# Optimization experiments

Measured on AMD Instinct MI355X. Metric: run time of the kernel, lower is better.

The kernel has to match this reference:

```python
import jax, jax.numpy as jnp
import numpy as np

B, T, E, H = 8, 4096, 1024, 128

def setup_inputs() -> dict:
    key = jax.random.key(0)
    kx, kq, kk, kv = jax.random.split(key, 4)
    x = jax.random.normal(kx, (B, T, E), dtype=jnp.float32)
    # bias-free Linear weights stored as (in, out) for x @ W
    scale = 1.0 / np.sqrt(E)
    Wq = jax.random.normal(kq, (E, H), dtype=jnp.float32) * scale
    Wk = jax.random.normal(kk, (E, H), dtype=jnp.float32) * scale
    Wv = jax.random.normal(kv, (E, H), dtype=jnp.float32) * scale
    return {"x": x, "Wq": Wq, "Wk": Wk, "Wv": Wv}

def reference(x, Wq, Wk, Wv):
    # x: (B,T,E) -> out: (B,T,H). Causal single-head attention, dropout p=0 (no-op).
    q = x @ Wq  # (B,T,H)
    k = x @ Wk
    v = x @ Wv
    head_norm = jnp.sqrt(jnp.float32(q.shape[-1]))
    att = jnp.einsum('bth,bsh->bts', q, k) / head_norm  # (B,T,T)
    causal = jnp.tril(jnp.ones((x.shape[1], x.shape[1]), dtype=bool))
    att = jnp.where(causal, att, -jnp.inf)
    att = jax.nn.softmax(att, axis=-1)
    return jnp.einsum('bts,bsh->bth', att, v)
```

## Files before the change

### kernel.cpp

```cpp
#include <hip/hip_runtime.h>
#include <hip/hip_bf16.h>
#include <stdint.h>

#define Bn 8
#define Tn 4096
#define En 1024
#define Hn 128
#define SCALE 0.08838834764831845f

typedef __attribute__((ext_vector_type(8))) short bf16x8;
typedef __attribute__((ext_vector_type(4))) float f32x4;

__device__ __forceinline__ float bf2f(unsigned short v) {
    return __uint_as_float(((unsigned int)v) << 16);
}
__device__ __forceinline__ unsigned int pkbf(float a, float b) {
    __hip_bfloat162 h = __float22bfloat162_rn(make_float2(a, b));
    union { __hip_bfloat162 h2; unsigned int u; } cv;
    cv.h2 = h;
    return cv.u;
}

__device__ __forceinline__ void gll16(const unsigned short* g, unsigned short* l) {
    __builtin_amdgcn_global_load_lds(
        (const __attribute__((address_space(1))) void*)g,
        (__attribute__((address_space(3))) void*)l, 16, 0, 0);
}

__global__ __launch_bounds__(256)
void qkv_mfma(const float* __restrict__ x,
              const float* __restrict__ Wq,
              const float* __restrict__ Wk,
              const float* __restrict__ Wv,
              unsigned short* __restrict__ Qo,
              unsigned short* __restrict__ Ko,
              unsigned short* __restrict__ Vo) {
    const int mt = blockIdx.x;
    const int which = blockIdx.y;
    const float* W = (which == 0) ? Wq : (which == 1) ? Wk : Wv;
    unsigned short* out = (which == 0) ? Qo : (which == 1) ? Ko : Vo;
    const float scale = (which == 0) ? SCALE : 1.0f;

    __shared__ alignas(16) unsigned short Xs[128 * 72];
    __shared__ alignas(16) unsigned short Wt[128 * 72];

    const int t = threadIdx.x;
    const int w = t >> 6;
    const int lane = t & 63;
    const int quad = lane >> 4;
    const int l16 = lane & 15;

    const int xrow = t >> 1;
    const int xkc = (t & 1) * 32;
    const int ws0 = (t & 31) * 2;
    const int wd0 = (t >> 5) * 16;

    const float* xsrc0 = x + (size_t)(mt * 128 + xrow) * En + xkc;

    f32x4 acc[2][8];
#pragma unroll
    for (int mi = 0; mi < 2; ++mi)
#pragma unroll
        for (int nst = 0; nst < 8; ++nst) acc[mi][nst] = (f32x4){0.f, 0.f, 0.f, 0.f};

    float4 xpre[8], wpre[8];
    {
        const float* src = xsrc0;
#pragma unroll
        for (int i = 0; i < 8; ++i) xpre[i] = *(const float4*)(src + i * 4);
        const float* w0 = W + (size_t)ws0 * Hn + wd0;
        const float* w1 = w0 + Hn;
#pragma unroll
        for (int i = 0; i < 4; ++i) wpre[i] = *(const float4*)(w0 + i * 4);
#pragma unroll
        for (int i = 0; i < 4; ++i) wpre[4 + i] = *(const float4*)(w1 + i * 4);
    }

    for (int kt = 0; kt < 16; ++kt) {
        __syncthreads();
        {
            unsigned int u[16];
#pragma unroll
            for (int i = 0; i < 8; ++i) {
                u[2 * i]     = pkbf(xpre[i].x, xpre[i].y);
                u[2 * i + 1] = pkbf(xpre[i].z, xpre[i].w);
            }
#pragma unroll
            for (int i = 0; i < 4; ++i)
                *(uint4*)&Xs[xrow * 72 + xkc + i * 8] = ((const uint4*)u)[i];

            const float* ax = (const float*)&wpre[0];
            const float* bx = (const float*)&wpre[4];
#pragma unroll
            for (int dd = 0; dd < 16; ++dd)
                *(unsigned int*)&Wt[(wd0 + dd) * 72 + ws0] = pkbf(ax[dd], bx[dd]);
        }
        if (kt < 15) {
            const float* src = xsrc0 + (kt + 1) * 64;
#pragma unroll
            for (int i = 0; i < 8; ++i) xpre[i] = *(const float4*)(src + i * 4);
            const float* w0 = W + (size_t)((kt + 1) * 64 + ws0) * Hn + wd0;
            const float* w1 = w0 + Hn;
#pragma unroll
            for (int i = 0; i < 4; ++i) wpre[i] = *(const float4*)(w0 + i * 4);
#pragma unroll
            for (int i = 0; i < 4; ++i) wpre[4 + i] = *(const float4*)(w1 + i * 4);
        }
        __syncthreads();

#pragma unroll
        for (int ks = 0; ks < 2; ++ks) {
            bf16x8 af[2];
#pragma unroll
            for (int mi = 0; mi < 2; ++mi)
                af[mi] = *(const bf16x8*)&Xs[(w * 32 + mi * 16 + l16) * 72 + ks * 32 + quad * 8];
#pragma unroll
            for (int nst = 0; nst < 8; ++nst) {
                bf16x8 bfr = *(const bf16x8*)&Wt[(nst * 16 + l16) * 72 + ks * 32 + quad * 8];
                acc[0][nst] = __builtin_amdgcn_mfma_f32_16x16x32_bf16(bfr, af[0], acc[0][nst], 0, 0, 0);
                acc[1][nst] = __builtin_amdgcn_mfma_f32_16x16x32_bf16(bfr, af[1], acc[1][nst], 0, 0, 0);
            }
        }
    }

#pragma unroll
    for (int mi = 0; mi < 2; ++mi) {
        const size_t rowbase = (size_t)(mt * 128 + w * 32 + mi * 16 + l16) * Hn;
#pragma unroll
        for (int nst = 0; nst < 8; ++nst) {
            f32x4 v = acc[mi][nst];
            uint2 pk;
            pk.x = pkbf(v[0] * scale, v[1] * scale);
            pk.y = pkbf(v[2] * scale, v[3] * scale);
            *(uint2*)(out + rowbase + nst * 16 + quad * 4) = pk;
        }
    }
}

#define KSWZ(r, c) (((r) << 8) + ((c) ^ (((r) & 7) << 4)))
#define VSWZ(r, c) (((r) << 7) + ((c) ^ (((r) & 7) << 4)))

__global__ __launch_bounds__(512, 4)
void flash_mfma(const unsigned short* __restrict__ Qb,
                const unsigned short* __restrict__ Kb,
                const unsigned short* __restrict__ Vb,
                float* __restrict__ out) {
    const int b = blockIdx.x;
    const int bx = blockIdx.y;
    const int qt = (bx < 32) ? (63 - bx) : (bx - 32);
    const int t = threadIdx.x;
    const int w = t >> 6;
    const int g = w >> 2;
    const int rg = w & 3;
    const int lane = t & 63;
    const int quad = lane >> 4;
    const int l16 = lane & 15;
    const int t256 = t & 255;

    extern __shared__ unsigned short pool[];
    char* const poolb = (char*)pool;
    char* const Kg = poolb + g * 16384;
    char* const Vg = poolb + 32768 + g * 16384;
    char* const Pw = poolb + 65536 + w * 2048;
    float* const Os = (float*)poolb;
    float* const Ex = (float*)(poolb + 40960);
    float* const Em = (float*)(poolb + 73728);
    float* const El = Em + 64;

    const size_t gbase = (size_t)b * ((size_t)Tn * Hn);
    const unsigned short* kbase = Kb + gbase;
    const unsigned short* vbase = Vb + gbase;

    const int l_hi = lane >> 4;
    const int cpr = (lane & 15) * 16;
    const int vs0 = (t256 & 31) * 2;
    const int vd0 = (t256 >> 5) * 16;

    uint4 vra, vrb, vrc, vrd;
    if (g <= qt) {
        const unsigned short* vsrc = vbase + (size_t)(g * 64) * Hn;
        vra = *(const uint4*)&vsrc[vs0 * 128 + vd0];
        vrb = *(const uint4*)&vsrc[vs0 * 128 + vd0 + 8];
        vrc = *(const uint4*)&vsrc[(vs0 + 1) * 128 + vd0];
        vrd = *(const uint4*)&vsrc[(vs0 + 1) * 128 + vd0 + 8];
    }

    {
        const unsigned short* qsrc = Qb + gbase + (size_t)(qt * 64) * Hn;
#pragma unroll
        for (int i = 0; i < 2; ++i) {
            const int row = w * 8 + i * 4 + l_hi;
            const int scol = cpr ^ ((row & 7) << 4);
            gll16(qsrc + row * 128 + (scol >> 1),
                  (unsigned short*)(poolb + w * 2048 + i * 1024));
        }
    }
    __syncthreads();

    bf16x8 qf[4];
#pragma unroll
    for (int ks = 0; ks < 4; ++ks)
        qf[ks] = *(const bf16x8*)(poolb + KSWZ(rg * 16 + l16, ks * 64 + quad * 16));

    f32x4 acc_o[8];
#pragma unroll
    for (int i = 0; i < 8; ++i) acc_o[i] = (f32x4){0.f, 0.f, 0.f, 0.f};
    float m_run = -1e30f, l_run = 0.f;

    const int n = (qt >> 1) + 1;
    for (int it = 0; it < n; ++it) {
        const int kt = 2 * it + g;
        const bool active = (kt <= qt);
        __syncthreads();
        if (active) {
            const unsigned short* ktile = kbase + (size_t)(kt * 64) * Hn;
#pragma unroll
            for (int i = 0; i < 4; ++i) {
                const int row = rg * 16 + i * 4 + l_hi;
                const int scol = cpr ^ ((row & 7) << 4);
                gll16(ktile + row * 128 + (scol >> 1),
                      (unsigned short*)(Kg + rg * 4096 + i * 1024));
            }
            const unsigned short* pa = (const unsigned short*)&vra;
            const unsigned short* pb = (const unsigned short*)&vrb;
            const unsigned short* pc = (const unsigned short*)&vrc;
            const unsigned short* pd = (const unsigned short*)&vrd;
#pragma unroll
            for (int dd = 0; dd < 8; ++dd)
                *(unsigned int*)(Vg + VSWZ(vd0 + dd, vs0 * 2)) =
                    (unsigned int)pa[dd] | ((unsigned int)pc[dd] << 16);
#pragma unroll
            for (int dd = 0; dd < 8; ++dd)
                *(unsigned int*)(Vg + VSWZ(vd0 + 8 + dd, vs0 * 2)) =
                    (unsigned int)pb[dd] | ((unsigned int)pd[dd] << 16);
        }
        __syncthreads();
        if (kt + 2 <= qt) {
            const unsigned short* vsrc = vbase + (size_t)((kt + 2) * 64) * Hn;
            vra = *(const uint4*)&vsrc[vs0 * 128 + vd0];
            vrb = *(const uint4*)&vsrc[vs0 * 128 + vd0 + 8];
            vrc = *(const uint4*)&vsrc[(vs0 + 1) * 128 + vd0];
            vrd = *(const uint4*)&vsrc[(vs0 + 1) * 128 + vd0 + 8];
        }
        if (!active) continue;

        const bool diag = (kt == qt);
        f32x4 sa[4];
#pragma unroll
        for (int st = 0; st < 4; ++st) {
            if (diag && st > rg) {
                sa[st] = (f32x4){-1e30f, -1e30f, -1e30f, -1e30f};
            } else {
                f32x4 c = (f32x4){0.f, 0.f, 0.f, 0.f};
#pragma unroll
                for (int ks = 0; ks < 4; ++ks) {
                    bf16x8 kf = *(const bf16x8*)(Kg + KSWZ(st * 16 + l16, ks * 64 + quad * 16));
                    c = __builtin_amdgcn_mfma_f32_16x16x32_bf16(kf, qf[ks], c, 0, 0, 0);
                }
                if (diag && st == rg) {
#pragma unroll
                    for (int r = 0; r < 4; ++r)
                        if (quad * 4 + r > l16) c[r] = -1e30f;
                }
                sa[st] = c;
            }
        }

        float mloc = -1e30f;
#pragma unroll
        for (int st = 0; st < 4; ++st)
#pragma unroll
            for (int r = 0; r < 4; ++r) mloc = fmaxf(mloc, sa[st][r]);
        mloc = fmaxf(mloc, __shfl_xor(mloc, 16));
        mloc = fmaxf(mloc, __shfl_xor(mloc, 32));
        const float m_new = fmaxf(m_run, mloc);
        const float alpha = __expf(m_run - m_new);
        float lsum = 0.f;
#pragma unroll
        for (int st = 0; st < 4; ++st)
#pragma unroll
            for (int r = 0; r < 4; ++r) {
                const float e = __expf(sa[st][r] - m_new);
                sa[st][r] = e;
                lsum += e;
            }
        lsum += __shfl_xor(lsum, 16);
        lsum += __shfl_xor(lsum, 32);
        l_run = l_run * alpha + lsum;
        m_run = m_new;
#pragma unroll
        for (int i = 0; i < 8; ++i) acc_o[i] *= alpha;

#pragma unroll
        for (int st = 0; st < 4; ++st) {
            uint2 pk;
            pk.x = pkbf(sa[st][0], sa[st][1]);
            pk.y = pkbf(sa[st][2], sa[st][3]);
            *(uint2*)(Pw + VSWZ(l16, st * 32 + quad * 8)) = pk;
        }
        bf16x8 pf0 = *(const bf16x8*)(Pw + VSWZ(l16, quad * 16));
        bf16x8 pf1 = *(const bf16x8*)(Pw + VSWZ(l16, 64 + quad * 16));

#pragma unroll
        for (int dt = 0; dt < 8; ++dt) {
            bf16x8 vf0 = *(const bf16x8*)(Vg + VSWZ(dt * 16 + l16, quad * 16));
            acc_o[dt] = __builtin_amdgcn_mfma_f32_16x16x32_bf16(vf0, pf0, acc_o[dt], 0, 0, 0);
            bf16x8 vf1 = *(const bf16x8*)(Vg + VSWZ(dt * 16 + l16, 64 + quad * 16));
            acc_o[dt] = __builtin_amdgcn_mfma_f32_16x16x32_bf16(vf1, pf1, acc_o[dt], 0, 0, 0);
        }
    }

    __syncthreads();
    if (g == 1) {
        float* dst = Ex + (rg * 16 + l16) * 128;
#pragma unroll
        for (int dt = 0; dt < 8; ++dt)
            *(f32x4*)&dst[dt * 16 + quad * 4] = acc_o[dt];
        if (quad == 0) {
            Em[rg * 16 + l16] = m_run;
            El[rg * 16 + l16] = l_run;
        }
    }
    __syncthreads();
    if (g == 0) {
        const float* src = Ex + (rg * 16 + l16) * 128;
        const float m2 = Em[rg * 16 + l16];
        const float l2 = El[rg * 16 + l16];
        const float ms = fmaxf(m_run, m2);
        const float a1 = __expf(m_run - ms);
        const float a2 = __expf(m2 - ms);
        const float linv = 1.f / (l_run * a1 + l2 * a2);
#pragma unroll
        for (int dt = 0; dt < 8; ++dt) {
            f32x4 o2 = *(const f32x4*)&src[dt * 16 + quad * 4];
            f32x4 v = (acc_o[dt] * a1 + o2 * a2) * linv;
            *(f32x4*)&Os[(rg * 16 + l16) * 132 + dt * 16 + quad * 4] = v;
        }
    }
    __syncthreads();
    float* dst = out + gbase + (size_t)(qt * 64) * Hn;
#pragma unroll
    for (int i = 0; i < 4; ++i) {
        const int idx = (t + i * 512) * 4;
        const int row = idx >> 7, col = idx & 127;
        *(float4*)&dst[row * 128 + col] = *(const float4*)&Os[row * 132 + col];
    }
}

extern "C" void kernel_launch(void* const* d_in, const int* in_sizes, int n_in,
                              void* d_out, int out_size, void* d_ws, size_t ws_size,
                              hipStream_t stream) {
    const float* x  = (const float*)d_in[0];
    const float* Wq = (const float*)d_in[1];
    const float* Wk = (const float*)d_in[2];
    const float* Wv = (const float*)d_in[3];
    float* o = (float*)d_out;

    unsigned short* Qb = (unsigned short*)d_ws;
    unsigned short* Kb = Qb + (size_t)Bn * Tn * Hn;
    unsigned short* Vb = Kb + (size_t)Bn * Tn * Hn;

    static bool attr_done = false;
    if (!attr_done) {
        hipFuncSetAttribute((const void*)flash_mfma,
                            hipFuncAttributeMaxDynamicSharedMemorySize, 81920);
        attr_done = true;
    }

    qkv_mfma<<<dim3(256, 3), 256, 0, stream>>>(x, Wq, Wk, Wv, Qb, Kb, Vb);
    flash_mfma<<<dim3(8, 64), 512, 81920, stream>>>(Qb, Kb, Vb, o);
}
```

Baseline: 369.8 us.

## Pre-convert x and weights to bf16 and use pipelined LDS-staged QKV GEMM

Adds separate kernels that convert x to bf16 and convert/transpose the projection weights once. A new QKV GEMM then reads bf16 tiles via direct global-to-LDS loads with XOR swizzle and double buffering. This is meant to cut redundant fp32 loads and in-kernel conversion across the three projection blocks, at the cost of an extra pass writing a bf16 copy of x, extra launches, and a larger workspace requirement with fallback to the old path.

```diff
diff --git a/kernel.cpp b/kernel.cpp
--- a/kernel.cpp
+++ b/kernel.cpp
@@ -25,6 +25,137 @@
     __builtin_amdgcn_global_load_lds(
         (const __attribute__((address_space(1))) void*)g,
         (__attribute__((address_space(3))) void*)l, 16, 0, 0);
+}
+
+__global__ __launch_bounds__(256)
+void xcvt(const float* __restrict__ x, unsigned short* __restrict__ xb) {
+    const size_t i = ((size_t)blockIdx.x * 256 + threadIdx.x) * 16;
+    const float4* src = (const float4*)(x + i);
+    float4 a = src[0], b = src[1], c = src[2], d = src[3];
+    uint4 o0, o1;
+    o0.x = pkbf(a.x, a.y); o0.y = pkbf(a.z, a.w);
+    o0.z = pkbf(b.x, b.y); o0.w = pkbf(b.z, b.w);
+    o1.x = pkbf(c.x, c.y); o1.y = pkbf(c.z, c.w);
+    o1.z = pkbf(d.x, d.y); o1.w = pkbf(d.z, d.w);
+    *(uint4*)(xb + i) = o0;
+    *(uint4*)(xb + i + 8) = o1;
+}
+
+__global__ __launch_bounds__(256)
+void wcvt(const float* __restrict__ Wq, const float* __restrict__ Wk,
+          const float* __restrict__ Wv, unsigned short* __restrict__ wt3) {
+    const int which = blockIdx.x;
+    const int k0 = blockIdx.y * 128;
+    const float* W = (which == 0) ? Wq : (which == 1) ? Wk : Wv;
+    unsigned short* wt = wt3 + (size_t)which * 131072;
+
+    __shared__ unsigned short wl[128 * 132];
+    const int t = threadIdx.x;
+#pragma unroll
+    for (int i = 0; i < 16; ++i) {
+        const int idx = t + i * 256;
+        const int k = idx >> 5, c4 = idx & 31;
+        float4 v = *(const float4*)&W[(size_t)(k0 + k) * Hn + c4 * 4];
+        uint2 p;
+        p.x = pkbf(v.x, v.y);
+        p.y = pkbf(v.z, v.w);
+        *(uint2*)&wl[k * 132 + c4 * 4] = p;
+    }
+    __syncthreads();
+#pragma unroll
+    for (int j = 0; j < 32; ++j) {
+        const int idx = t + j * 256;
+        const int n = idx >> 6, kp = idx & 63;
+        unsigned int u = (unsigned int)wl[(2 * kp) * 132 + n] |
+                         ((unsigned int)wl[(2 * kp + 1) * 132 + n] << 16);
+        *(unsigned int*)&wt[(size_t)n * 1024 + k0 + 2 * kp] = u;
+    }
+}
+
+#define QSWZ(r, c) (((r) << 7) + ((c) ^ (((r) & 7) << 4)))
+
+__global__ __launch_bounds__(256)
+void qkv2(const unsigned short* __restrict__ xb,
+          const unsigned short* __restrict__ wt3,
+          unsigned short* __restrict__ Qo,
+          unsigned short* __restrict__ Ko,
+          unsigned short* __restrict__ Vo) {
+    const int mt = blockIdx.x;
+    const int which = blockIdx.y;
+    const unsigned short* wt = wt3 + (size_t)which * 131072;
+    unsigned short* out = (which == 0) ? Qo : (which == 1) ? Ko : Vo;
+    const float scale = (which == 0) ? SCALE : 1.0f;
+
+    __shared__ alignas(16) unsigned short Xs[2][128 * 64];
+    __shared__ alignas(16) unsigned short Ws[2][128 * 64];
+
+    const int t = threadIdx.x;
+    const int w = t >> 6;
+    const int lane = t & 63;
+    const int quad = lane >> 4;
+    const int l16 = lane & 15;
+    const int r8 = lane >> 3;
+    const int cb = lane & 7;
+
+    const unsigned short* xtile = xb + (size_t)(mt * 128) * En;
+
+    f32x4 acc[2][8];
+#pragma unroll
+    for (int mi = 0; mi < 2; ++mi)
+#pragma unroll
+        for (int nst = 0; nst < 8; ++nst) acc[mi][nst] = (f32x4){0.f, 0.f, 0.f, 0.f};
+
+    auto stage = [&](int buf, int kt) {
+#pragma unroll
+        for (int i = 0; i < 4; ++i) {
+            const int row = i * 32 + w * 8 + r8;
+            gll16(xtile + (size_t)row * En + kt * 64 + ((cb ^ (row & 7)) * 8),
+                  &Xs[buf][(i * 32 + w * 8) * 64]);
+        }
+#pragma unroll
+        for (int i = 0; i < 4; ++i) {
+            const int row = i * 32 + w * 8 + r8;
+            gll16(wt + (size_t)row * 1024 + kt * 64 + ((cb ^ (row & 7)) * 8),
+                  &Ws[buf][(i * 32 + w * 8) * 64]);
+        }
+    };
+
+    stage(0, 0);
+    __syncthreads();
+
+    for (int kt = 0; kt < 16; ++kt) {
+        const int buf = kt & 1;
+        if (kt < 15) stage(buf ^ 1, kt + 1);
+        const char* xs = (const char*)Xs[buf];
+        const char* ws = (const char*)Ws[buf];
+#pragma unroll
+        for (int ks = 0; ks < 2; ++ks) {
+            bf16x8 af[2];
+#pragma unroll
+            for (int mi = 0; mi < 2; ++mi)
+                af[mi] = *(const bf16x8*)(xs + QSWZ(w * 32 + mi * 16 + l16, ks * 64 + quad * 16));
+#pragma unroll
+            for (int nst = 0; nst < 8; ++nst) {
+                bf16x8 bfr = *(const bf16x8*)(ws + QSWZ(nst * 16 + l16, ks * 64 + quad * 16));
+                acc[0][nst] = __builtin_amdgcn_mfma_f32_16x16x32_bf16(bfr, af[0], acc[0][nst], 0, 0, 0);
+                acc[1][nst] = __builtin_amdgcn_mfma_f32_16x16x32_bf16(bfr, af[1], acc[1][nst], 0, 0, 0);
+            }
+        }
+        if (kt < 15) __syncthreads();
+    }
+
+#pragma unroll
+    for (int mi = 0; mi < 2; ++mi) {
+        const size_t rowbase = (size_t)(mt * 128 + w * 32 + mi * 16 + l16) * Hn;
+#pragma unroll
+        for (int nst = 0; nst < 8; ++nst) {
+            f32x4 v = acc[mi][nst];
+            uint2 pk;
+            pk.x = pkbf(v[0] * scale, v[1] * scale);
+            pk.y = pkbf(v[2] * scale, v[3] * scale);
+            *(uint2*)(out + rowbase + nst * 16 + quad * 4) = pk;
+        }
+    }
 }
 
 __global__ __launch_bounds__(256)
@@ -356,9 +487,15 @@
     const float* Wv = (const float*)d_in[3];
     float* o = (float*)d_out;
 
+    const size_t qkvb = (size_t)Bn * Tn * Hn;
     unsigned short* Qb = (unsigned short*)d_ws;
-    unsigned short* Kb = Qb + (size_t)Bn * Tn * Hn;
-    unsigned short* Vb = Kb + (size_t)Bn * Tn * Hn;
+    unsigned short* Kb = Qb + qkvb;
+    unsigned short* Vb = Kb + qkvb;
+    unsigned short* xbf = Vb + qkvb;
+    unsigned short* wt3 = xbf + (size_t)Bn * Tn * En;
+
+    const size_t ws_need = (3 * qkvb + (size_t)Bn * Tn * En + 3 * (size_t)Hn * En)
+                           * sizeof(unsigned short);
 
     static bool attr_done = false;
     if (!attr_done) {
@@ -367,6 +504,12 @@
         attr_done = true;
     }
 
-    qkv_mfma<<<dim3(256, 3), 256, 0, stream>>>(x, Wq, Wk, Wv, Qb, Kb, Vb);
+    if (ws_size >= ws_need) {
+        xcvt<<<8192, 256, 0, stream>>>(x, xbf);
+        wcvt<<<dim3(3, 8), 256, 0, stream>>>(Wq, Wk, Wv, wt3);
+        qkv2<<<dim3(256, 3), 256, 0, stream>>>(xbf, wt3, Qb, Kb, Vb);
+    } else {
+        qkv_mfma<<<dim3(256, 3), 256, 0, stream>>>(x, Wq, Wk, Wv, Qb, Kb, Vb);
+    }
     flash_mfma<<<dim3(8, 64), 512, 81920, stream>>>(Qb, Kb, Vb, o);
 }
```

Result: faster. 356.5 us (-3.6%).
